# Kernel tuning notes

Measured on AMD Instinct MI355X. Metric: run time of the kernel, lower is better.

Reference implementation:

```python
import jax, jax.numpy as jnp
import numpy as np

# Hyperparameters (from init_kwargs)
N = 100000      # num_nodes
T = 4           # num_edge_type
E = 400000      # edges per type
C = 2           # num_channels
L = 2           # num_layers
W_IN = 128      # input feature dim
D = 64          # node_dim (w_out)
NUM_CLASS = 16
BETA = 0.5
M = 10000       # number of target nodes


def setup_inputs() -> dict:
    key = jax.random.key(0)
    ks = jax.random.split(key, 10)
    glorot = np.sqrt(6.0 / (W_IN + D))
    glorot1 = np.sqrt(6.0 / (C * D + D))
    glorot2 = np.sqrt(6.0 / (D + NUM_CLASS))
    return {
        "X": jax.random.normal(ks[0], (N, W_IN), dtype=jnp.float32),
        "edge_value": jax.random.uniform(ks[1], (T, E), dtype=jnp.float32),
        "conv_weights": 0.1 * jax.random.normal(ks[2], (L, C, T), dtype=jnp.float32),
        "Ws": jax.random.uniform(ks[3], (C, W_IN, D), minval=-glorot, maxval=glorot, dtype=jnp.float32),
        "lin1_w": jax.random.uniform(ks[4], (C * D, D), minval=-glorot1, maxval=glorot1, dtype=jnp.float32),
        "lin1_b": jnp.zeros((D,), dtype=jnp.float32),
        "lin_w": jax.random.uniform(ks[5], (D, NUM_CLASS), minval=-glorot2, maxval=glorot2, dtype=jnp.float32),
        "lin_b": jnp.zeros((NUM_CLASS,), dtype=jnp.float32),
        "edge_index": jax.random.randint(ks[6], (T, 2, E), 0, N),
        "target_x": jax.random.randint(ks[7], (M,), 0, N),
    }


def reference(X, edge_value, conv_weights, Ws, lin1_w, lin1_b, lin_w, lin_b,
              edge_index, target_x):
    # Flatten edge types into one big edge list. torch_sparse.coalesce(op='add')
    # followed by torch.sparse.mm is mathematically a duplicate-summing SpMM,
    # i.e. a segment_sum over destination rows.
    rows = edge_index[:, 0, :].reshape(-1)      # [T*E]
    cols = edge_index[:, 1, :].reshape(-1)      # [T*E]
    vals = edge_value.reshape(-1)               # [T*E]
    type_id = jnp.repeat(jnp.arange(T), E)      # [T*E] edge-type id (constant)

    # Per-channel input projections: X_ = X @ Ws[c]  -> [C, N, D]
    X_ = jnp.einsum('nf,cfd->cnd', X, Ws)
    H = X_

    for l in range(L):
        # FastGTConv: softmax over edge types per channel
        filt = jax.nn.softmax(conv_weights[l], axis=1)   # [C, T]
        newH = []
        for c in range(C):
            v = vals * filt[c, type_id]                  # [T*E] mixed edge weights
            msgs = v[:, None] * H[c][cols]               # gather + scale: [T*E, D]
            newH.append(jax.ops.segment_sum(msgs, rows, num_segments=N))
        H = jnp.stack(newH)                              # [C, N, D]

    # FastGTN tail: relu(beta*X_ + (1-beta)*H), concat channels, linear1
    Hc = jax.nn.relu(BETA * X_ + (1.0 - BETA) * H)       # [C, N, D]
    Hcat = jnp.transpose(Hc, (1, 0, 2)).reshape(N, C * D)
    H_ = Hcat @ lin1_w + lin1_b                          # [N, D]

    # FastGTNs head: logits at target nodes
    return H_[target_x] @ lin_w + lin_b                  # [M, NUM_CLASS]
```

## Files before the change

kernel.cpp:

```cpp
#include <hip/hip_runtime.h>

#define N_NODES   100000
#define T_TYPES   4
#define E_EDGES   400000
#define E4        100000
#define G_TOT     400000
#define TE_TOT    1600000
#define C_CH      2
#define L_LAYERS  2
#define W_INF     128
#define DD        64
#define NUM_CLASS 16
#define BETA      0.5f
#define M_TGT     10000

#define NBKT      391
#define BROWS     256
#define BPAD      4864
#define CHUNK_G   1024
#define NPART_BLK 391
#define PROJ_BLK  1563

static const size_t PLANE2 = (size_t)N_NODES * DD;

typedef __attribute__((ext_vector_type(8))) short short8x;
typedef __attribute__((ext_vector_type(4))) float f32x4;

__device__ __forceinline__ unsigned bf16rne(float x) {
    unsigned u = __float_as_uint(x);
    return (u + 0x7FFFu + ((u >> 16) & 1u)) >> 16;
}
__device__ __forceinline__ unsigned packbf(float a, float b) {
    return bf16rne(a) | (bf16rne(b) << 16);
}
__device__ __forceinline__ float bflo(unsigned u) { return __uint_as_float(u << 16); }
__device__ __forceinline__ float bfhi(unsigned u) { return __uint_as_float(u & 0xFFFF0000u); }

__device__ __forceinline__ void load_filter(const float* cw, int layer,
                                            float* f0, float* f1) {
    float m0 = -1e30f, m1 = -1e30f;
    #pragma unroll
    for (int t = 0; t < T_TYPES; ++t) {
        f0[t] = cw[layer * C_CH * T_TYPES + t];
        f1[t] = cw[layer * C_CH * T_TYPES + T_TYPES + t];
        m0 = fmaxf(m0, f0[t]); m1 = fmaxf(m1, f1[t]);
    }
    float s0 = 0.f, s1 = 0.f;
    #pragma unroll
    for (int t = 0; t < T_TYPES; ++t) {
        f0[t] = __expf(f0[t] - m0); s0 += f0[t];
        f1[t] = __expf(f1[t] - m1); s1 += f1[t];
    }
    #pragma unroll
    for (int t = 0; t < T_TYPES; ++t) { f0[t] /= s0; f1[t] /= s1; }
}

__global__ void prep_kernel(const float* __restrict__ Ws,
                            unsigned short* __restrict__ Wsb,
                            int* __restrict__ cursor) {
    int b = blockIdx.x;
    int tid = threadIdx.x;
    if (b < 64) {
        int idx = b * 256 + tid;
        int c   = idx >> 13;
        int rem = idx & 8191;
        int d   = rem >> 7;
        int k   = rem & 127;
        Wsb[idx] = (unsigned short)bf16rne(Ws[c * (W_INF * DD) + k * DD + d]);
    } else {
        int idx = (b - 64) * 256 + tid;
        if (idx < NBKT) cursor[idx] = idx * BPAD;
    }
}

#define AROW 136
#define SMEM_BYTES 45664

__global__ __launch_bounds__(256) void build_proj_kernel(
        const int* __restrict__ edge_index,
        const float* __restrict__ edge_value,
        const float* __restrict__ cw,
        int* __restrict__ cursor,
        int2* __restrict__ edata2,
        const float* __restrict__ X,
        const unsigned short* __restrict__ Wsb,
        unsigned* __restrict__ Xp16) {
    __shared__ __align__(16) char smem[SMEM_BYTES];
    int tid = threadIdx.x;

    if (blockIdx.x < NPART_BLK) {
        int* cnt   = (int*)smem;
        int* lbase = cnt + 392;
        int* gbase = lbase + 392;
        int2* le   = (int2*)(smem + 4704);
        unsigned short* lbk = (unsigned short*)(smem + 4704 + 32768);

        int p = blockIdx.x;
        for (int j = tid; j < NBKT; j += 256) cnt[j] = 0;
        __syncthreads();

        float f0[T_TYPES], f1[T_TYPES];
        load_filter(cw, 0, f0, f1);

        int px[16], pv[16], rk[16], bk[16];
        int ne = 0;
        #pragma unroll
        for (int g = 0; g < 4; ++g) {
            int idx = p * CHUNK_G + g * 256 + tid;
            if (idx < G_TOT) {
                int t = idx / E4, r = idx - t * E4;
                const int* bptr = edge_index + (size_t)t * 2 * E_EDGES;
                int4   rw = ((const int4*)bptr)[r];
                int4   cl = ((const int4*)(bptr + E_EDGES))[r];
                float4 vv = ((const float4*)(edge_value + (size_t)t * E_EDGES))[r];
                int tb = t << 17;
                int   rr[4] = {rw.x, rw.y, rw.z, rw.w};
                int   cc[4] = {cl.x, cl.y, cl.z, cl.w};
                float vf[4] = {vv.x, vv.y, vv.z, vv.w};
                #pragma unroll
                for (int k = 0; k < 4; ++k) {
                    int b = rr[k] >> 8;
                    px[ne] = cc[k] | tb | ((rr[k] & 255) << 19);
                    pv[ne] = __float_as_int(vf[k]);
                    bk[ne] = b;
                    rk[ne] = atomicAdd(&cnt[b], 1);
                    ++ne;
                }
            }
        }
        __syncthreads();
        if (tid < 64) {
            int c[7]; int s = 0;
            #pragma unroll
            for (int k = 0; k < 7; ++k) {
                int idx = tid * 7 + k;
                c[k] = (idx < NBKT) ? cnt[idx] : 0;
                s += c[k];
            }
            int inc = s;
            #pragma unroll
            for (int off = 1; off < 64; off <<= 1) {
                int v = __shfl_up(inc, off);
                if (tid >= off) inc += v;
            }
            int base = inc - s;
            #pragma unroll
            for (int k = 0; k < 7; ++k) {
                int idx = tid * 7 + k;
                if (idx < NBKT) lbase[idx] = base;
                base += c[k];
            }
        }
        __syncthreads();
        #pragma unroll
        for (int k = 0; k < 16; ++k) {
            if (k < ne) {
                int slot = lbase[bk[k]] + rk[k];
                le[slot]  = make_int2(px[k], pv[k]);
                lbk[slot] = (unsigned short)bk[k];
            }
        }
        __syncthreads();
        for (int j = tid; j < NBKT; j += 256)
            gbase[j] = cnt[j] ? atomicAdd(&cursor[j], cnt[j]) : 0;
        __syncthreads();
        int ngrp = min(CHUNK_G, G_TOT - p * CHUNK_G);
        int nloc = 4 * ngrp;
        for (int j = tid; j < nloc; j += 256) {
            int b = lbk[j];
            int2 e = le[j];
            int t = (e.x >> 17) & 3;
            float v = __int_as_float(e.y);
            edata2[gbase[b] + (j - lbase[b])] =
                make_int2(e.x, (int)packbf(v * f0[t], v * f1[t]));
        }
    } else {
        unsigned short* a_lds = (unsigned short*)smem;
        int row0 = (blockIdx.x - NPART_BLK) * 64;

        const float4* X4 = (const float4*)X;
        #pragma unroll
        for (int i = 0; i < 8; ++i) {
            int gi = tid + 256 * i;
            int r  = gi >> 5;
            int c4 = gi & 31;
            int row = row0 + r;
            float4 v = make_float4(0.f, 0.f, 0.f, 0.f);
            if (row < N_NODES) v = X4[(size_t)row * 32 + c4];
            *(uint2*)&a_lds[r * AROW + c4 * 4] = make_uint2(packbf(v.x, v.y),
                                                            packbf(v.z, v.w));
        }
        __syncthreads();

        int wave = tid >> 6, lane = tid & 63;
        int m = lane & 15, q = lane >> 4;

        short8x A[4];
        #pragma unroll
        for (int ks = 0; ks < 4; ++ks)
            A[ks] = *(const short8x*)&a_lds[(wave * 16 + m) * AROW + ks * 32 + q * 8];

        #pragma unroll
        for (int ct = 0; ct < 4; ++ct) {
            f32x4 acc0 = {0.f, 0.f, 0.f, 0.f};
            f32x4 acc1 = {0.f, 0.f, 0.f, 0.f};
            #pragma unroll
            for (int ks = 0; ks < 4; ++ks) {
                short8x B0 = *(const short8x*)(Wsb + (ct * 16 + m) * 128 + ks * 32 + q * 8);
                short8x B1 = *(const short8x*)(Wsb + 8192 + (ct * 16 + m) * 128 + ks * 32 + q * 8);
                acc0 = __builtin_amdgcn_mfma_f32_16x16x32_bf16(A[ks], B0, acc0, 0, 0, 0);
                acc1 = __builtin_amdgcn_mfma_f32_16x16x32_bf16(A[ks], B1, acc1, 0, 0, 0);
            }
            #pragma unroll
            for (int r = 0; r < 4; ++r) {
                int row = row0 + wave * 16 + q * 4 + r;
                if (row < N_NODES)
                    Xp16[(size_t)row * DD + ct * 16 + m] = packbf(acc0[r], acc1[r]);
            }
        }
    }
}

__global__ __launch_bounds__(512) void rowsort_kernel(const int* __restrict__ cursor,
                                                      int2* __restrict__ edata2,
                                                      int* __restrict__ offs) {
    __shared__ int rcnt[BROWS];
    __shared__ int rbase[BROWS];
    __shared__ int rcur[BROWS];
    __shared__ int2 le[BPAD];
    int b   = blockIdx.x;
    int tid = threadIdx.x;
    int bb  = b * BPAD;
    int cnt = cursor[b] - bb;
    if (tid < BROWS) rcnt[tid] = 0;
    __syncthreads();
    for (int j = tid; j < cnt; j += 512) {
        int2 e = edata2[bb + j];
        le[j] = e;
        atomicAdd(&rcnt[(e.x >> 19) & 255], 1);
    }
    __syncthreads();
    if (tid < 64) {
        int c[4]; int s = 0;
        #pragma unroll
        for (int k = 0; k < 4; ++k) { c[k] = rcnt[tid * 4 + k]; s += c[k]; }
        int inc = s;
        #pragma unroll
        for (int off = 1; off < 64; off <<= 1) {
            int v = __shfl_up(inc, off);
            if (tid >= off) inc += v;
        }
        int base = inc - s;
        #pragma unroll
        for (int k = 0; k < 4; ++k) { rbase[tid * 4 + k] = base; base += c[k]; }
    }
    __syncthreads();
    if (tid < BROWS) rcur[tid] = rbase[tid];
    __syncthreads();
    for (int j = tid; j < cnt; j += 512) {
        int2 e = le[j];
        int lr = (e.x >> 19) & 255;
        int pos = atomicAdd(&rcur[lr], 1);
        edata2[bb + pos] = e;
    }
    int row0  = b * BROWS;
    int nrows = min(BROWS, N_NODES - row0);
    if (tid < nrows)
        offs[row0 + tid] = bb + rbase[tid] + rcnt[tid];
}

__device__ __forceinline__ void qfma(const uint4 h, unsigned wp,
                                     float4& a, float4& b) {
    float w0 = bflo(wp), w1 = bfhi(wp);
    a.x = fmaf(w0, bflo(h.x), a.x);
    a.y = fmaf(w1, bfhi(h.x), a.y);
    a.z = fmaf(w0, bflo(h.y), a.z);
    a.w = fmaf(w1, bfhi(h.y), a.w);
    b.x = fmaf(w0, bflo(h.z), b.x);
    b.y = fmaf(w1, bfhi(h.z), b.y);
    b.z = fmaf(w0, bflo(h.w), b.z);
    b.w = fmaf(w1, bfhi(h.w), b.w);
}

__device__ __forceinline__ void qreduce(float4& a, float4& b) {
    a.x += __shfl_xor(a.x, 16); a.y += __shfl_xor(a.y, 16);
    a.z += __shfl_xor(a.z, 16); a.w += __shfl_xor(a.w, 16);
    b.x += __shfl_xor(b.x, 16); b.y += __shfl_xor(b.y, 16);
    b.z += __shfl_xor(b.z, 16); b.w += __shfl_xor(b.w, 16);
    a.x += __shfl_xor(a.x, 32); a.y += __shfl_xor(a.y, 32);
    a.z += __shfl_xor(a.z, 32); a.w += __shfl_xor(a.w, 32);
    b.x += __shfl_xor(b.x, 32); b.y += __shfl_xor(b.y, 32);
    b.z += __shfl_xor(b.z, 32); b.w += __shfl_xor(b.w, 32);
}

__device__ __forceinline__ int row_beg(const int* offs, int row) {
    return ((row & 255) == 0) ? (row >> 8) * BPAD : offs[row - 1];
}

__global__ __launch_bounds__(256) void spmm_gather(const unsigned* __restrict__ Hin16,
                                                   unsigned* __restrict__ Hout16,
                                                   const int* __restrict__ offs,
                                                   const int2* __restrict__ edata2) {
    int lane = threadIdx.x & 63;
    int s16 = lane & 15, sub = lane >> 4;
    int row  = (blockIdx.x * blockDim.x + threadIdx.x) >> 6;
    int beg = row_beg(offs, row);
    int end = offs[row];
    const uint4* hp = (const uint4*)Hin16;
    float4 a = make_float4(0.f, 0.f, 0.f, 0.f);
    float4 b = make_float4(0.f, 0.f, 0.f, 0.f);
    int i = beg + sub;
    for (; i + 4 < end; i += 8) {
        int2 e0 = edata2[i];
        int2 e1 = edata2[i + 4];
        uint4 h0 = hp[(size_t)(e0.x & 0x1FFFF) * 16 + s16];
        uint4 h1 = hp[(size_t)(e1.x & 0x1FFFF) * 16 + s16];
        qfma(h0, (unsigned)e0.y, a, b);
        qfma(h1, (unsigned)e1.y, a, b);
    }
    if (i < end) {
        int2 e = edata2[i];
        uint4 h = hp[(size_t)(e.x & 0x1FFFF) * 16 + s16];
        qfma(h, (unsigned)e.y, a, b);
    }
    qreduce(a, b);
    if (sub == 0)
        ((uint4*)Hout16)[(size_t)row * 16 + s16] =
            make_uint4(packbf(a.x, a.y), packbf(a.z, a.w),
                       packbf(b.x, b.y), packbf(b.z, b.w));
}

__global__ __launch_bounds__(256) void tgt_tail_kernel(const unsigned* __restrict__ Hin16,
                                                       const unsigned* __restrict__ Xp16,
                                                       const int* __restrict__ offs,
                                                       const int2* __restrict__ edata2,
                                                       const float* __restrict__ cw,
                                                       const int* __restrict__ tgt,
                                                       const float* __restrict__ lin1_w,
                                                       const float* __restrict__ lin1_b,
                                                       const float* __restrict__ lin_w,
                                                       const float* __restrict__ lin_b,
                                                       float* __restrict__ out) {
    __shared__ float l1w[W_INF * DD];
    __shared__ float lw[DD * NUM_CLASS];
    __shared__ float l1b[DD];
    __shared__ float lb[NUM_CLASS];
    __shared__ float hc[4][W_INF];
    __shared__ float hmid[4][DD];

    int tid = threadIdx.x;
    {
        const float4* g = (const float4*)lin1_w;
        float4* s = (float4*)l1w;
        #pragma unroll
        for (int i = 0; i < 8; ++i) s[tid + 256 * i] = g[tid + 256 * i];
        ((float4*)lw)[tid] = ((const float4*)lin_w)[tid];
        if (tid < DD) l1b[tid] = lin1_b[tid];
        else if (tid < DD + NUM_CLASS) lb[tid - DD] = lin_b[tid - DD];
    }

    float f0a[T_TYPES], f1a[T_TYPES], f0b[T_TYPES], f1b[T_TYPES];
    load_filter(cw, 0, f0a, f1a);
    load_filter(cw, 1, f0b, f1b);
    float r0[T_TYPES], r1[T_TYPES];
    #pragma unroll
    for (int t = 0; t < T_TYPES; ++t) { r0[t] = f0b[t] / f0a[t]; r1[t] = f1b[t] / f1a[t]; }

    int w = tid >> 6, lane = tid & 63;
    int s16 = lane & 15, sub = lane >> 4;
    int m = blockIdx.x * 4 + w;
    int row = tgt[m];
    int beg = row_beg(offs, row);
    int end = offs[row];
    const uint4* hp = (const uint4*)Hin16;
    float4 a = make_float4(0.f, 0.f, 0.f, 0.f);
    float4 b = make_float4(0.f, 0.f, 0.f, 0.f);
    for (int i = beg + sub; i < end; i += 4) {
        int2 e = edata2[i];
        int t = (e.x >> 17) & 3;
        uint4 h = hp[(size_t)(e.x & 0x1FFFF) * 16 + s16];
        unsigned wp = (unsigned)e.y;
        float w0 = bflo(wp) * r0[t], w1 = bfhi(wp) * r1[t];
        a.x = fmaf(w0, bflo(h.x), a.x);
        a.y = fmaf(w1, bfhi(h.x), a.y);
        a.z = fmaf(w0, bflo(h.y), a.z);
        a.w = fmaf(w1, bfhi(h.y), a.w);
        b.x = fmaf(w0, bflo(h.z), b.x);
        b.y = fmaf(w1, bfhi(h.z), b.y);
        b.z = fmaf(w0, bflo(h.w), b.z);
        b.w = fmaf(w1, bfhi(h.w), b.w);
    }
    qreduce(a, b);

    if (sub == 0) {
        uint4 xu = ((const uint4*)Xp16)[(size_t)row * 16 + s16];
        int d0 = 4 * s16;
        hc[w][d0 + 0]      = fmaxf(BETA * bflo(xu.x) + (1.f - BETA) * a.x, 0.f);
        hc[w][DD + d0 + 0] = fmaxf(BETA * bfhi(xu.x) + (1.f - BETA) * a.y, 0.f);
        hc[w][d0 + 1]      = fmaxf(BETA * bflo(xu.y) + (1.f - BETA) * a.z, 0.f);
        hc[w][DD + d0 + 1] = fmaxf(BETA * bfhi(xu.y) + (1.f - BETA) * a.w, 0.f);
        hc[w][d0 + 2]      = fmaxf(BETA * bflo(xu.z) + (1.f - BETA) * b.x, 0.f);
        hc[w][DD + d0 + 2] = fmaxf(BETA * bfhi(xu.z) + (1.f - BETA) * b.y, 0.f);
        hc[w][d0 + 3]      = fmaxf(BETA * bflo(xu.w) + (1.f - BETA) * b.z, 0.f);
        hc[w][DD + d0 + 3] = fmaxf(BETA * bfhi(xu.w) + (1.f - BETA) * b.w, 0.f);
    }
    __syncthreads();

    float a1 = l1b[lane];
    #pragma unroll 8
    for (int k = 0; k < W_INF; ++k)
        a1 = fmaf(hc[w][k], l1w[k * DD + lane], a1);
    hmid[w][lane] = a1;
    __syncthreads();

    if (lane < NUM_CLASS) {
        float o = lb[lane];
        #pragma unroll 8
        for (int k = 0; k < DD; ++k)
            o = fmaf(hmid[w][k], lw[k * NUM_CLASS + lane], o);
        out[(size_t)m * NUM_CLASS + lane] = o;
    }
}

extern "C" void kernel_launch(void* const* d_in, const int* in_sizes, int n_in,
                              void* d_out, int out_size, void* d_ws, size_t ws_size,
                              hipStream_t stream) {
    const float* X            = (const float*)d_in[0];
    const float* edge_value   = (const float*)d_in[1];
    const float* conv_weights = (const float*)d_in[2];
    const float* Ws           = (const float*)d_in[3];
    const float* lin1_w       = (const float*)d_in[4];
    const float* lin1_b       = (const float*)d_in[5];
    const float* lin_w        = (const float*)d_in[6];
    const float* lin_b        = (const float*)d_in[7];
    const int*   edge_index   = (const int*)d_in[8];
    const int*   target_x     = (const int*)d_in[9];
    float* out = (float*)d_out;

    unsigned*       Xp16 = (unsigned*)d_ws;
    unsigned*       H116 = Xp16 + PLANE2;
    unsigned short* Wsb  = (unsigned short*)(H116 + PLANE2);
    int*            offs = (int*)(Wsb + C_CH * W_INF * DD);
    int*            cursor = offs + N_NODES;
    int2*           edata2 = (int2*)(cursor + 512);

    prep_kernel<<<66, 256, 0, stream>>>(Ws, Wsb, cursor);
    build_proj_kernel<<<NPART_BLK + PROJ_BLK, 256, 0, stream>>>(
        edge_index, edge_value, conv_weights, cursor, edata2, X, Wsb, Xp16);
    rowsort_kernel<<<NBKT, 512, 0, stream>>>(cursor, edata2, offs);
    spmm_gather<<<(N_NODES * 64) / 256, 256, 0, stream>>>(Xp16, H116, offs, edata2);
    tgt_tail_kernel<<<M_TGT / 4, 256, 0, stream>>>(H116, Xp16, offs, edata2,
                                                   conv_weights, target_x,
                                                   lin1_w, lin1_b, lin_w, lin_b, out);
}
```

Measured before the change: 253.0 us.

## Halve row-bucket size and split fused partition/projection kernel into two

Edge partitioning now uses 782 buckets of 128 rows, with smaller per-block chunks and a smaller per-bucket pad. The row sort runs with 256-thread blocks over smaller buckets, which should cut LDS use and raise occupancy. The fused partition-plus-projection kernel is split into separate partition and MFMA projection kernels, so each uses its own shared-memory footprint. This costs one extra kernel launch and loses any overlap between the two halves of the old fused launch.

```diff
diff --git a/kernel.cpp b/kernel.cpp
--- a/kernel.cpp
+++ b/kernel.cpp
@@ -14,12 +14,11 @@
 #define BETA      0.5f
 #define M_TGT     10000
 
-#define NBKT      391
-#define BROWS     256
-#define BPAD      4864
-#define CHUNK_G   1024
-#define NPART_BLK 391
-#define PROJ_BLK  1563
+#define NBKT      782
+#define BROWS     128
+#define BPAD      2560
+#define CHUNK_G   512
+#define NPART_BLK 782
 
 static const size_t PLANE2 = (size_t)N_NODES * DD;
 
@@ -73,155 +72,150 @@
     }
 }
 
+__global__ __launch_bounds__(256) void partition_kernel(const int* __restrict__ edge_index,
+                                                        const float* __restrict__ edge_value,
+                                                        const float* __restrict__ cw,
+                                                        int* __restrict__ cursor,
+                                                        int2* __restrict__ edata2) {
+    __shared__ int cnt[NBKT];
+    __shared__ int lbase[NBKT];
+    __shared__ int gbase[NBKT];
+    __shared__ int2 le[CHUNK_G * 4];
+    __shared__ unsigned short lbk[CHUNK_G * 4];
+    int tid = threadIdx.x;
+    for (int j = tid; j < NBKT; j += 256) cnt[j] = 0;
+    __syncthreads();
+
+    float f0[T_TYPES], f1[T_TYPES];
+    load_filter(cw, 0, f0, f1);
+
+    int px[8], pv[8], rk[8], bk[8];
+    int ne = 0;
+    #pragma unroll
+    for (int g = 0; g < 2; ++g) {
+        int idx = blockIdx.x * CHUNK_G + g * 256 + tid;
+        if (idx < G_TOT) {
+            int t = idx / E4, r = idx - t * E4;
+            const int* bptr = edge_index + (size_t)t * 2 * E_EDGES;
+            int4   rw = ((const int4*)bptr)[r];
+            int4   cl = ((const int4*)(bptr + E_EDGES))[r];
+            float4 vv = ((const float4*)(edge_value + (size_t)t * E_EDGES))[r];
+            int tb = t << 17;
+            int   rr[4] = {rw.x, rw.y, rw.z, rw.w};
+            int   cc[4] = {cl.x, cl.y, cl.z, cl.w};
+            float vf[4] = {vv.x, vv.y, vv.z, vv.w};
+            #pragma unroll
+            for (int k = 0; k < 4; ++k) {
+                int b = rr[k] >> 7;
+                px[ne] = cc[k] | tb | ((rr[k] & 127) << 19);
+                pv[ne] = __float_as_int(vf[k]);
+                bk[ne] = b;
+                rk[ne] = atomicAdd(&cnt[b], 1);
+                ++ne;
+            }
+        }
+    }
+    __syncthreads();
+    if (tid < 64) {
+        int c[13]; int s = 0;
+        #pragma unroll
+        for (int k = 0; k < 13; ++k) {
+            int idx = tid * 13 + k;
+            c[k] = (idx < NBKT) ? cnt[idx] : 0;
+            s += c[k];
+        }
+        int inc = s;
+        #pragma unroll
+        for (int off = 1; off < 64; off <<= 1) {
+            int v = __shfl_up(inc, off);
+            if (tid >= off) inc += v;
+        }
+        int base = inc - s;
+        #pragma unroll
+        for (int k = 0; k < 13; ++k) {
+            int idx = tid * 13 + k;
+            if (idx < NBKT) lbase[idx] = base;
+            base += c[k];
+        }
+    }
+    __syncthreads();
+    #pragma unroll
+    for (int k = 0; k < 8; ++k) {
+        if (k < ne) {
+            int slot = lbase[bk[k]] + rk[k];
+            le[slot]  = make_int2(px[k], pv[k]);
+            lbk[slot] = (unsigned short)bk[k];
+        }
+    }
+    __syncthreads();
+    for (int j = tid; j < NBKT; j += 256) {
+        int c = cnt[j];
+        gbase[j] = c ? atomicAdd(&cursor[j], c) : 0;
+    }
+    __syncthreads();
+    int ngrp = min(CHUNK_G, G_TOT - blockIdx.x * CHUNK_G);
+    int nloc = 4 * ngrp;
+    for (int j = tid; j < nloc; j += 256) {
+        int b = lbk[j];
+        int2 e = le[j];
+        int t = (e.x >> 17) & 3;
+        float v = __int_as_float(e.y);
+        edata2[gbase[b] + (j - lbase[b])] =
+            make_int2(e.x, (int)packbf(v * f0[t], v * f1[t]));
+    }
+}
+
 #define AROW 136
-#define SMEM_BYTES 45664
-
-__global__ __launch_bounds__(256) void build_proj_kernel(
-        const int* __restrict__ edge_index,
-        const float* __restrict__ edge_value,
-        const float* __restrict__ cw,
-        int* __restrict__ cursor,
-        int2* __restrict__ edata2,
-        const float* __restrict__ X,
-        const unsigned short* __restrict__ Wsb,
-        unsigned* __restrict__ Xp16) {
-    __shared__ __align__(16) char smem[SMEM_BYTES];
-    int tid = threadIdx.x;
-
-    if (blockIdx.x < NPART_BLK) {
-        int* cnt   = (int*)smem;
-        int* lbase = cnt + 392;
-        int* gbase = lbase + 392;
-        int2* le   = (int2*)(smem + 4704);
-        unsigned short* lbk = (unsigned short*)(smem + 4704 + 32768);
-
-        int p = blockIdx.x;
-        for (int j = tid; j < NBKT; j += 256) cnt[j] = 0;
-        __syncthreads();
-
-        float f0[T_TYPES], f1[T_TYPES];
-        load_filter(cw, 0, f0, f1);
-
-        int px[16], pv[16], rk[16], bk[16];
-        int ne = 0;
-        #pragma unroll
-        for (int g = 0; g < 4; ++g) {
-            int idx = p * CHUNK_G + g * 256 + tid;
-            if (idx < G_TOT) {
-                int t = idx / E4, r = idx - t * E4;
-                const int* bptr = edge_index + (size_t)t * 2 * E_EDGES;
-                int4   rw = ((const int4*)bptr)[r];
-                int4   cl = ((const int4*)(bptr + E_EDGES))[r];
-                float4 vv = ((const float4*)(edge_value + (size_t)t * E_EDGES))[r];
-                int tb = t << 17;
-                int   rr[4] = {rw.x, rw.y, rw.z, rw.w};
-                int   cc[4] = {cl.x, cl.y, cl.z, cl.w};
-                float vf[4] = {vv.x, vv.y, vv.z, vv.w};
-                #pragma unroll
-                for (int k = 0; k < 4; ++k) {
-                    int b = rr[k] >> 8;
-                    px[ne] = cc[k] | tb | ((rr[k] & 255) << 19);
-                    pv[ne] = __float_as_int(vf[k]);
-                    bk[ne] = b;
-                    rk[ne] = atomicAdd(&cnt[b], 1);
-                    ++ne;
-                }
-            }
-        }
-        __syncthreads();
-        if (tid < 64) {
-            int c[7]; int s = 0;
-            #pragma unroll
-            for (int k = 0; k < 7; ++k) {
-                int idx = tid * 7 + k;
-                c[k] = (idx < NBKT) ? cnt[idx] : 0;
-                s += c[k];
-            }
-            int inc = s;
-            #pragma unroll
-            for (int off = 1; off < 64; off <<= 1) {
-                int v = __shfl_up(inc, off);
-                if (tid >= off) inc += v;
-            }
-            int base = inc - s;
-            #pragma unroll
-            for (int k = 0; k < 7; ++k) {
-                int idx = tid * 7 + k;
-                if (idx < NBKT) lbase[idx] = base;
-                base += c[k];
-            }
-        }
-        __syncthreads();
-        #pragma unroll
-        for (int k = 0; k < 16; ++k) {
-            if (k < ne) {
-                int slot = lbase[bk[k]] + rk[k];
-                le[slot]  = make_int2(px[k], pv[k]);
-                lbk[slot] = (unsigned short)bk[k];
-            }
-        }
-        __syncthreads();
-        for (int j = tid; j < NBKT; j += 256)
-            gbase[j] = cnt[j] ? atomicAdd(&cursor[j], cnt[j]) : 0;
-        __syncthreads();
-        int ngrp = min(CHUNK_G, G_TOT - p * CHUNK_G);
-        int nloc = 4 * ngrp;
-        for (int j = tid; j < nloc; j += 256) {
-            int b = lbk[j];
-            int2 e = le[j];
-            int t = (e.x >> 17) & 3;
-            float v = __int_as_float(e.y);
-            edata2[gbase[b] + (j - lbase[b])] =
-                make_int2(e.x, (int)packbf(v * f0[t], v * f1[t]));
-        }
-    } else {
-        unsigned short* a_lds = (unsigned short*)smem;
-        int row0 = (blockIdx.x - NPART_BLK) * 64;
-
-        const float4* X4 = (const float4*)X;
-        #pragma unroll
-        for (int i = 0; i < 8; ++i) {
-            int gi = tid + 256 * i;
-            int r  = gi >> 5;
-            int c4 = gi & 31;
-            int row = row0 + r;
-            float4 v = make_float4(0.f, 0.f, 0.f, 0.f);
-            if (row < N_NODES) v = X4[(size_t)row * 32 + c4];
-            *(uint2*)&a_lds[r * AROW + c4 * 4] = make_uint2(packbf(v.x, v.y),
-                                                            packbf(v.z, v.w));
-        }
-        __syncthreads();
-
-        int wave = tid >> 6, lane = tid & 63;
-        int m = lane & 15, q = lane >> 4;
-
-        short8x A[4];
-        #pragma unroll
-        for (int ks = 0; ks < 4; ++ks)
-            A[ks] = *(const short8x*)&a_lds[(wave * 16 + m) * AROW + ks * 32 + q * 8];
-
-        #pragma unroll
-        for (int ct = 0; ct < 4; ++ct) {
-            f32x4 acc0 = {0.f, 0.f, 0.f, 0.f};
-            f32x4 acc1 = {0.f, 0.f, 0.f, 0.f};
-            #pragma unroll
-            for (int ks = 0; ks < 4; ++ks) {
-                short8x B0 = *(const short8x*)(Wsb + (ct * 16 + m) * 128 + ks * 32 + q * 8);
-                short8x B1 = *(const short8x*)(Wsb + 8192 + (ct * 16 + m) * 128 + ks * 32 + q * 8);
-                acc0 = __builtin_amdgcn_mfma_f32_16x16x32_bf16(A[ks], B0, acc0, 0, 0, 0);
-                acc1 = __builtin_amdgcn_mfma_f32_16x16x32_bf16(A[ks], B1, acc1, 0, 0, 0);
-            }
-            #pragma unroll
-            for (int r = 0; r < 4; ++r) {
-                int row = row0 + wave * 16 + q * 4 + r;
-                if (row < N_NODES)
-                    Xp16[(size_t)row * DD + ct * 16 + m] = packbf(acc0[r], acc1[r]);
-            }
-        }
-    }
-}
-
-__global__ __launch_bounds__(512) void rowsort_kernel(const int* __restrict__ cursor,
+__global__ __launch_bounds__(256) void proj_mfma(const float* __restrict__ X,
+                                                 const unsigned short* __restrict__ Wsb,
+                                                 unsigned* __restrict__ Xp16) {
+    __shared__ unsigned short a_lds[64 * AROW];
+    int tid  = threadIdx.x;
+    int row0 = blockIdx.x * 64;
+
+    const float4* X4 = (const float4*)X;
+    #pragma unroll
+    for (int i = 0; i < 8; ++i) {
+        int gi = tid + 256 * i;
+        int r  = gi >> 5;
+        int c4 = gi & 31;
+        int row = row0 + r;
+        float4 v = make_float4(0.f, 0.f, 0.f, 0.f);
+        if (row < N_NODES) v = X4[(size_t)row * 32 + c4];
+        *(uint2*)&a_lds[r * AROW + c4 * 4] = make_uint2(packbf(v.x, v.y),
+                                                        packbf(v.z, v.w));
+    }
+    __syncthreads();
+
+    int wave = tid >> 6, lane = tid & 63;
+    int m = lane & 15, q = lane >> 4;
+
+    short8x A[4];
+    #pragma unroll
+    for (int ks = 0; ks < 4; ++ks)
+        A[ks] = *(const short8x*)&a_lds[(wave * 16 + m) * AROW + ks * 32 + q * 8];
+
+    #pragma unroll
+    for (int ct = 0; ct < 4; ++ct) {
+        f32x4 acc0 = {0.f, 0.f, 0.f, 0.f};
+        f32x4 acc1 = {0.f, 0.f, 0.f, 0.f};
+        #pragma unroll
+        for (int ks = 0; ks < 4; ++ks) {
+            short8x B0 = *(const short8x*)(Wsb + (ct * 16 + m) * 128 + ks * 32 + q * 8);
+            short8x B1 = *(const short8x*)(Wsb + 8192 + (ct * 16 + m) * 128 + ks * 32 + q * 8);
+            acc0 = __builtin_amdgcn_mfma_f32_16x16x32_bf16(A[ks], B0, acc0, 0, 0, 0);
+            acc1 = __builtin_amdgcn_mfma_f32_16x16x32_bf16(A[ks], B1, acc1, 0, 0, 0);
+        }
+        #pragma unroll
+        for (int r = 0; r < 4; ++r) {
+            int row = row0 + wave * 16 + q * 4 + r;
+            if (row < N_NODES)
+                Xp16[(size_t)row * DD + ct * 16 + m] = packbf(acc0[r], acc1[r]);
+        }
+    }
+}
+
+__global__ __launch_bounds__(256) void rowsort_kernel(const int* __restrict__ cursor,
                                                       int2* __restrict__ edata2,
                                                       int* __restrict__ offs) {
     __shared__ int rcnt[BROWS];
@@ -234,16 +228,15 @@
     int cnt = cursor[b] - bb;
     if (tid < BROWS) rcnt[tid] = 0;
     __syncthreads();
-    for (int j = tid; j < cnt; j += 512) {
+    for (int j = tid; j < cnt; j += 256) {
         int2 e = edata2[bb + j];
         le[j] = e;
-        atomicAdd(&rcnt[(e.x >> 19) & 255], 1);
+        atomicAdd(&rcnt[(e.x >> 19) & 127], 1);
     }
     __syncthreads();
     if (tid < 64) {
-        int c[4]; int s = 0;
-        #pragma unroll
-        for (int k = 0; k < 4; ++k) { c[k] = rcnt[tid * 4 + k]; s += c[k]; }
+        int c0 = rcnt[tid * 2], c1 = rcnt[tid * 2 + 1];
+        int s = c0 + c1;
         int inc = s;
         #pragma unroll
         for (int off = 1; off < 64; off <<= 1) {
@@ -251,15 +244,15 @@
             if (tid >= off) inc += v;
         }
         int base = inc - s;
-        #pragma unroll
-        for (int k = 0; k < 4; ++k) { rbase[tid * 4 + k] = base; base += c[k]; }
+        rbase[tid * 2]     = base;
+        rbase[tid * 2 + 1] = base + c0;
     }
     __syncthreads();
     if (tid < BROWS) rcur[tid] = rbase[tid];
     __syncthreads();
-    for (int j = tid; j < cnt; j += 512) {
+    for (int j = tid; j < cnt; j += 256) {
         int2 e = le[j];
-        int lr = (e.x >> 19) & 255;
+        int lr = (e.x >> 19) & 127;
         int pos = atomicAdd(&rcur[lr], 1);
         edata2[bb + pos] = e;
     }
@@ -294,7 +287,7 @@
 }
 
 __device__ __forceinline__ int row_beg(const int* offs, int row) {
-    return ((row & 255) == 0) ? (row >> 8) * BPAD : offs[row - 1];
+    return ((row & 127) == 0) ? (row >> 7) * BPAD : offs[row - 1];
 }
 
 __global__ __launch_bounds__(256) void spmm_gather(const unsigned* __restrict__ Hin16,
@@ -442,12 +435,13 @@
     unsigned short* Wsb  = (unsigned short*)(H116 + PLANE2);
     int*            offs = (int*)(Wsb + C_CH * W_INF * DD);
     int*            cursor = offs + N_NODES;
-    int2*           edata2 = (int2*)(cursor + 512);
-
-    prep_kernel<<<66, 256, 0, stream>>>(Ws, Wsb, cursor);
-    build_proj_kernel<<<NPART_BLK + PROJ_BLK, 256, 0, stream>>>(
-        edge_index, edge_value, conv_weights, cursor, edata2, X, Wsb, Xp16);
-    rowsort_kernel<<<NBKT, 512, 0, stream>>>(cursor, edata2, offs);
+    int2*           edata2 = (int2*)(cursor + 1024);
+
+    prep_kernel<<<68, 256, 0, stream>>>(Ws, Wsb, cursor);
+    partition_kernel<<<NPART_BLK, 256, 0, stream>>>(edge_index, edge_value,
+                                                    conv_weights, cursor, edata2);
+    proj_mfma<<<(N_NODES + 63) / 64, 256, 0, stream>>>(X, Wsb, Xp16);
+    rowsort_kernel<<<NBKT, 256, 0, stream>>>(cursor, edata2, offs);
     spmm_gather<<<(N_NODES * 64) / 256, 256, 0, stream>>>(Xp16, H116, offs, edata2);
     tgt_tail_kernel<<<M_TGT / 4, 256, 0, stream>>>(H116, Xp16, offs, edata2,
                                                    conv_weights, target_x,
```

New measurement: 268.6 us. 1.06x slower.
